# Kernel optimization log

Measured on AMD Instinct MI355X. Metric: run time of the kernel, lower is better.

## Reference

```python
import jax, jax.numpy as jnp
import numpy as np
from jax import lax

FILTERS = 8

def _conv(x, k):
    # x: (B,H,W,Cin), k: (KH,KW,Cin,Cout), SAME padding, stride 1
    return lax.conv_general_dilated(x, k, (1, 1), 'SAME',
                                    dimension_numbers=('NHWC', 'HWIO', 'NHWC'))

def _hard_sigmoid(x):
    # keras hard_sigmoid: clip(0.2*x + 0.5, 0, 1)
    return jnp.clip(0.2 * x + 0.5, 0.0, 1.0)


def setup_inputs() -> dict:
    key = jax.random.key(0)
    ks = jax.random.split(key, 4)
    B, T, H, W, C = 32, 16, 64, 64, 3
    x = jax.random.normal(ks[0], (B, T, H, W, C), dtype=jnp.float32)
    W_x = jax.random.normal(ks[1], (3, 3, C, 4 * FILTERS), dtype=jnp.float32) * 0.1
    W_h = jax.random.normal(ks[2], (3, 3, FILTERS, 4 * FILTERS), dtype=jnp.float32) * 0.1
    b = jnp.zeros((4 * FILTERS,), dtype=jnp.float32)
    W_out = jax.random.normal(ks[3], (H * W * FILTERS, 4), dtype=jnp.float32) * 0.02
    b_out = jnp.zeros((4,), dtype=jnp.float32)
    return {"x": x, "W_x": W_x, "W_h": W_h, "b": b, "W_out": W_out, "b_out": b_out}


def reference(x, W_x, W_h, b, W_out, b_out):
    B, T, H, W, C = x.shape
    F = FILTERS

    def step(carry, xt):
        h, c = carry
        z = _conv(xt, W_x) + _conv(h, W_h) + b  # (B,H,W,4F)
        zi, zf, zc, zo = jnp.split(z, 4, axis=-1)  # keras gate order: i, f, c, o
        i = _hard_sigmoid(zi)
        f = _hard_sigmoid(zf)
        c = f * c + i * jnp.tanh(zc)
        o = _hard_sigmoid(zo)
        h = o * jnp.tanh(c)
        return (h, c), None

    h0 = jnp.zeros((B, H, W, F), dtype=x.dtype)
    c0 = jnp.zeros((B, H, W, F), dtype=x.dtype)
    xs = jnp.moveaxis(x, 1, 0)  # (T,B,H,W,C)
    (h_final, _), _ = lax.scan(step, (h0, c0), xs)

    flat = h_final.reshape(B, -1)  # (B, H*W*F)
    logits = flat @ W_out + b_out
    return jax.nn.softmax(logits, axis=-1)
```

## Files before the change

kernel.cpp:

```cpp
#include <hip/hip_runtime.h>
#include <math.h>

#define NB 32
#define NT 16

typedef _Float16 f16;
typedef _Float16 half2f __attribute__((ext_vector_type(2)));
typedef _Float16 half4f __attribute__((ext_vector_type(4)));
typedef _Float16 half8f __attribute__((ext_vector_type(8)));
typedef float    floatx2 __attribute__((ext_vector_type(2)));
typedef float    floatx4 __attribute__((ext_vector_type(4)));

#define XPAD_OFF  0u
#define HPAD0_OFF 18382848u
#define HPAD1_OFF 20680704u
#define CBUF_OFF  22978560u
#define WBQ_OFF   27172864u
#define PART_OFF  27181056u
#define WS_NEED   27197440u

#define BANDA   0
#define BANDB   15232
#define CLDS4   30464
#define REDF4   55040
#define SMEM5   55296

__device__ __forceinline__ float hard_sigmoid(float v) {
    return fminf(fmaxf(fmaf(0.2f, v, 0.5f), 0.0f), 1.0f);
}
__device__ __forceinline__ float fast_tanh(float v) {
    float e = __builtin_amdgcn_exp2f(v * 2.8853900817779268f);
    return 1.0f - 2.0f * __builtin_amdgcn_rcpf(e + 1.0f);
}

__device__ __forceinline__ float wb_entry(int i, const float* Wx,
                                          const float* Wh, const float* bias) {
    int e = i & 7, l = (i >> 3) & 63, n = (i >> 9) & 1, j = i >> 10;
    int h = l >> 4;
    int rr = l & 15;
    int g = (rr & 3) * 8 + 2 * (rr >> 2) + n;
    float wv = 0.f;
    if (j == 0) {
        wv = Wh[(h * 8 + e) * 32 + g];
    } else if (j == 1) {
        wv = Wh[((4 + h) * 8 + e) * 32 + g];
    } else if (j == 2 && h == 0) {
        wv = Wh[(64 + e) * 32 + g];
    } else if (j == 3 && h == 3) {
        wv = (e == 3) ? bias[g] : 0.f;
    } else {
        int ty, txp;
        if (j == 2) { ty = (h == 3) ? 1 : 0; txp = (h == 2) ? 2 : 0; }
        else        { ty = (h == 0) ? 1 : 2; txp = (h == 1) ? 0 : 2; }
        int txq = txp + (e >> 2), c = e & 3;
        if (txq < 3 && c < 3)
            wv = Wx[((ty * 3 + txq) * 3 + c) * 32 + g];
    }
    return wv;
}

#define LDX(base, off) ({                                                  \
    half4f lo_ = *(const half4f*)((base) + (off));                         \
    half4f hi_ = *(const half4f*)((base) + (off) + 8);                     \
    __builtin_shufflevector(lo_, hi_, 0, 1, 2, 3, 4, 5, 6, 7); })

#define GATE_BODY(A0, A1, A2, A3, COLD0, COLD1, CC0, CC1, HH0, HH1)        \
    {                                                                      \
        floatx4 acc0 = {0.f, 0.f, 0.f, 0.f};                               \
        floatx4 acc1 = {0.f, 0.f, 0.f, 0.f};                               \
        acc0 = __builtin_amdgcn_mfma_f32_16x16x32_f16(B00, A0, acc0,0,0,0);\
        acc1 = __builtin_amdgcn_mfma_f32_16x16x32_f16(B01, A0, acc1,0,0,0);\
        acc0 = __builtin_amdgcn_mfma_f32_16x16x32_f16(B10, A1, acc0,0,0,0);\
        acc1 = __builtin_amdgcn_mfma_f32_16x16x32_f16(B11, A1, acc1,0,0,0);\
        acc0 = __builtin_amdgcn_mfma_f32_16x16x32_f16(B20, A2, acc0,0,0,0);\
        acc1 = __builtin_amdgcn_mfma_f32_16x16x32_f16(B21, A2, acc1,0,0,0);\
        acc0 = __builtin_amdgcn_mfma_f32_16x16x32_f16(B30, A3, acc0,0,0,0);\
        acc1 = __builtin_amdgcn_mfma_f32_16x16x32_f16(B31, A3, acc1,0,0,0);\
        float ig0 = hard_sigmoid(acc0[0]), fg0 = hard_sigmoid(acc0[1]);    \
        float cg0 = fast_tanh(acc0[2]),    og0 = hard_sigmoid(acc0[3]);    \
        CC0 = fmaf(fg0, COLD0, ig0 * cg0);                                 \
        HH0 = og0 * fast_tanh(CC0);                                        \
        float ig1 = hard_sigmoid(acc1[0]), fg1 = hard_sigmoid(acc1[1]);    \
        float cg1 = fast_tanh(acc1[2]),    og1 = hard_sigmoid(acc1[3]);    \
        CC1 = fmaf(fg1, COLD1, ig1 * cg1);                                 \
        HH1 = og1 * fast_tanh(CC1);                                        \
    }

__global__ __launch_bounds__(256) void init_all(
    const float* __restrict__ x,
    const float* __restrict__ Wx, const float* __restrict__ Wh,
    const float* __restrict__ bias,
    f16* __restrict__ xpad, f16* __restrict__ h0, f16* __restrict__ h1,
    f16* __restrict__ WB)
{
    int i = blockIdx.x * 256 + threadIdx.x;
    if (i < 200704) {
        int bt = i / 392, p = i - bt * 392;
        int rr, cc;
        if (p < 136) { rr = (p < 68) ? 0 : 65; cc = p - ((p < 68) ? 0 : 68); }
        else { int q = p - 136; rr = 1 + (q >> 2); int m = q & 3;
               cc = (m == 0) ? 0 : 64 + m; }
        half4f v = {0, 0, 0, (f16)1.0f};
        *(half4f*)(xpad + ((size_t)(bt * 66 + rr) * 68 + cc) * 4) = v;
    } else if (i < 225792) {
        int k = i - 200704;
        int buf = k / 12544; k -= buf * 12544;
        int b = k / 392, p = k - b * 392;
        int rr, cc;
        if (p < 136) { rr = (p < 68) ? 0 : 65; cc = p - ((p < 68) ? 0 : 68); }
        else { int q = p - 136; rr = 1 + (q >> 2); int m = q & 3;
               cc = (m == 0) ? 0 : 64 + m; }
        f16* hp = buf ? h1 : h0;
        half8f zz = {0, 0, 0, 0, 0, 0, 0, 0};
        *(half8f*)(hp + ((size_t)(b * 66 + rr) * 68 + cc) * 8) = zz;
    } else if (i < 229888) {
        int k = i - 225792;
        WB[k] = (f16)wb_entry(k, Wx, Wh, bias);
    } else if (i < 754176) {
        int j = i - 229888;
        int b = j >> 14;
        int rem = j & 16383;
        int s = rem >> 12, px = rem & 4095;
        const float* xp = x + ((size_t)(b * 16 + s) * 4096 + px) * 3;
        half4f v = {(f16)xp[0], (f16)xp[1], (f16)xp[2], (f16)1.0f};
        int gr = px >> 6, gc = px & 63;
        *(half4f*)(xpad + ((size_t)((b * 16 + s) * 66 + gr + 1) * 68 + gc + 1) * 4) = v;
    }
}

__global__ __launch_bounds__(1024, 4) void convlstm_fused4w(
    const float* __restrict__ x,
    f16* __restrict__ xpad,
    const f16* __restrict__ WB,
    const f16* __restrict__ h_in,
    f16* __restrict__ h_out,
    float* __restrict__ c_buf,
    const float* __restrict__ Wout,
    float* __restrict__ partial,
    int t, int first, int do_head)
{
    __shared__ __attribute__((aligned(16))) char smem[SMEM5];

    const int bid0 = blockIdx.x;
    const int bid  = ((bid0 & 7) << 5) | (bid0 >> 3);
    const int bi  = bid >> 3;
    const int r0  = (bid & 7) << 3;
    const int tid = threadIdx.x;
    const int w    = __builtin_amdgcn_readfirstlane(tid >> 6);
    const int lane = tid & 63;
    const int p16  = lane & 15;
    const int g4   = lane >> 4;
    const int f0   = g4 << 1;

    const int csl = t + 4 + (tid >> 8);
    const bool cv = (csl < NT);
    const int cpb = (tid & 255) << 1;
    const int cgr = r0 + (cpb >> 6), cgc = cpb & 63;
    float cxa0 = 0.f, cxa1 = 0.f, cxa2 = 0.f;
    float cxb0 = 0.f, cxb1 = 0.f, cxb2 = 0.f;
    if (cv) {
        const float* p = x + ((size_t)(bi * NT + csl) * 4096 + cgr * 64 + cgc) * 3;
        cxa0 = p[0]; cxa1 = p[1]; cxa2 = p[2];
        cxb0 = p[3]; cxb1 = p[4]; cxb2 = p[5];
    }

    const half8f* WBv = (const half8f*)WB;
    half8f B00 = WBv[0*64+lane], B01 = WBv[1*64+lane];
    half8f B10 = WBv[2*64+lane], B11 = WBv[3*64+lane];
    half8f B20 = WBv[4*64+lane], B21 = WBv[5*64+lane];
    half8f B30 = WBv[6*64+lane], B31 = WBv[7*64+lane];

    const int ty0 = (g4 >= 3) ? 1 : 0, tx0 = g4 - 3 * ty0;
    const int ty1 = 1 + ((g4 >= 2) ? 1 : 0), tx1 = (g4 + 4) - 3 * ty1;
    const int ty2 = (g4 == 3) ? 1 : 0, tx2 = (g4 == 2) ? 2 : 0;
    const int ty3 = (g4 == 0) ? 1 : 2, tx3 = (g4 == 1) ? 0 : 2;

    const half8f z8 = {0, 0, 0, 0, 0, 0, 0, 0};

    if (tid < 56) {
        int buf = tid / 28;
        int r2  = (tid % 28) >> 1;
        int cc  = (tid & 1) ? 65 : 0;
        *(half8f*)(smem + (buf ? BANDB : BANDA) + (r2 * 68 + cc) * 16) = z8;
    }

    #pragma unroll
    for (int k = 0; k < 4; ++k) {
        const int tau = k * 16 + w;
        if (tau < 56) {
            const int bl = tau >> 2, ct = tau & 3;
            const int row = r0 - 3 + bl;
            const bool vA = ((unsigned)row < 64u);
            const int colA = ct * 16 + p16;
            float cc0 = 0.f, cc1 = 0.f, hh0 = 0.f, hh1 = 0.f;
            if (vA) {
                floatx2 cold = {0.f, 0.f};
                if (!first)
                    cold = *(const floatx2*)(c_buf +
                               ((size_t)(bi * 4096 + row * 64 + colA)) * 8 + f0);
                const char* hpA = (const char*)(h_in + ((size_t)(bi * 66 + row)) * 68 * 8);
                const char* xpA = (const char*)(xpad +
                    ((size_t)((bi * 16 + t) * 66 + row)) * 68 * 4);
                half8f a0 = first ? z8 : *(const half8f*)(hpA + (ty0 * 68 + colA + tx0) * 16);
                half8f a1 = first ? z8 : *(const half8f*)(hpA + (ty1 * 68 + colA + tx1) * 16);
                half8f a2;
                if (g4 == 0) a2 = first ? z8 : *(const half8f*)(hpA + (2 * 68 + colA + 2) * 16);
                else         a2 = LDX(xpA, (ty2 * 68 + colA + tx2) * 8);
                half8f a3 = LDX(xpA, (ty3 * 68 + colA + tx3) * 8);
                GATE_BODY(a0, a1, a2, a3, cold[0], cold[1], cc0, cc1, hh0, hh1);
            }
            half2f hw = {(f16)hh0, (f16)hh1};
            *(half2f*)(smem + BANDA + (bl * 68 + 1 + colA) * 16 + f0 * 2) = hw;
            if (bl >= 1 && bl <= 12) {
                floatx2 cw = {cc0, cc1};
                *(floatx2*)(smem + CLDS4 + (((bl - 1) * 64 + colA) * 8 + f0) * 4) = cw;
            }
        }
    }
    __syncthreads();

    #pragma unroll
    for (int k = 0; k < 3; ++k) {
        const int tau = k * 16 + w;
        const int bl = 1 + (tau >> 2), ct = tau & 3;
        const int row = r0 - 3 + bl;
        const bool vA = ((unsigned)row < 64u);
        const int colA = ct * 16 + p16;
        float cc0 = 0.f, cc1 = 0.f, hh0 = 0.f, hh1 = 0.f;
        if (vA) {
            floatx2 cold = *(const floatx2*)(smem + CLDS4 +
                               (((bl - 1) * 64 + colA) * 8 + f0) * 4);
            const char* xpA = (const char*)(xpad +
                ((size_t)((bi * 16 + t + 1) * 66 + row)) * 68 * 4);
            half8f a0 = *(const half8f*)(smem + BANDA + ((bl - 1 + ty0) * 68 + colA + tx0) * 16);
            half8f a1 = *(const half8f*)(smem + BANDA + ((bl - 1 + ty1) * 68 + colA + tx1) * 16);
            half8f a2;
            if (g4 == 0) a2 = *(const half8f*)(smem + BANDA + ((bl + 1) * 68 + colA + 2) * 16);
            else         a2 = LDX(xpA, (ty2 * 68 + colA + tx2) * 8);
            half8f a3 = LDX(xpA, (ty3 * 68 + colA + tx3) * 8);
            GATE_BODY(a0, a1, a2, a3, cold[0], cold[1], cc0, cc1, hh0, hh1);
        }
        half2f hw = {(f16)hh0, (f16)hh1};
        *(half2f*)(smem + BANDB + (bl * 68 + 1 + colA) * 16 + f0 * 2) = hw;
        floatx2 cw = {cc0, cc1};
        *(floatx2*)(smem + CLDS4 + (((bl - 1) * 64 + colA) * 8 + f0) * 4) = cw;
    }
    __syncthreads();

    #pragma unroll
    for (int k = 0; k < 3; ++k) {
        const int tau = k * 16 + w;
        if (tau < 40) {
            const int bl = 2 + (tau >> 2), ct = tau & 3;
            const int row = r0 - 3 + bl;
            const bool vA = ((unsigned)row < 64u);
            const int colA = ct * 16 + p16;
            float cc0 = 0.f, cc1 = 0.f, hh0 = 0.f, hh1 = 0.f;
            if (vA) {
                floatx2 cold = *(const floatx2*)(smem + CLDS4 +
                                   (((bl - 1) * 64 + colA) * 8 + f0) * 4);
                const char* xpA = (const char*)(xpad +
                    ((size_t)((bi * 16 + t + 2) * 66 + row)) * 68 * 4);
                half8f a0 = *(const half8f*)(smem + BANDB + ((bl - 1 + ty0) * 68 + colA + tx0) * 16);
                half8f a1 = *(const half8f*)(smem + BANDB + ((bl - 1 + ty1) * 68 + colA + tx1) * 16);
                half8f a2;
                if (g4 == 0) a2 = *(const half8f*)(smem + BANDB + ((bl + 1) * 68 + colA + 2) * 16);
                else         a2 = LDX(xpA, (ty2 * 68 + colA + tx2) * 8);
                half8f a3 = LDX(xpA, (ty3 * 68 + colA + tx3) * 8);
                GATE_BODY(a0, a1, a2, a3, cold[0], cold[1], cc0, cc1, hh0, hh1);
            }
            half2f hw = {(f16)hh0, (f16)hh1};
            *(half2f*)(smem + BANDA + (bl * 68 + 1 + colA) * 16 + f0 * 2) = hw;
            floatx2 cw = {cc0, cc1};
            *(floatx2*)(smem + CLDS4 + (((bl - 1) * 64 + colA) * 8 + f0) * 4) = cw;
        }
    }
    __syncthreads();

    {
        float ha0 = 0.f, ha1 = 0.f, ha2 = 0.f, ha3 = 0.f;
        #pragma unroll
        for (int k = 0; k < 2; ++k) {
            const int tau = k * 16 + w;
            const int bl = 3 + (tau >> 2), ct = tau & 3;
            const int row = r0 - 3 + bl;
            const int colA = ct * 16 + p16;
            floatx2 cold = *(const floatx2*)(smem + CLDS4 +
                               (((bl - 1) * 64 + colA) * 8 + f0) * 4);
            const char* xpA = (const char*)(xpad +
                ((size_t)((bi * 16 + t + 3) * 66 + row)) * 68 * 4);
            half8f a0 = *(const half8f*)(smem + BANDA + ((bl - 1 + ty0) * 68 + colA + tx0) * 16);
            half8f a1 = *(const half8f*)(smem + BANDA + ((bl - 1 + ty1) * 68 + colA + tx1) * 16);
            half8f a2;
            if (g4 == 0) a2 = *(const half8f*)(smem + BANDA + ((bl + 1) * 68 + colA + 2) * 16);
            else         a2 = LDX(xpA, (ty2 * 68 + colA + tx2) * 8);
            half8f a3 = LDX(xpA, (ty3 * 68 + colA + tx3) * 8);
            float cc0, cc1, hh0, hh1;
            GATE_BODY(a0, a1, a2, a3, cold[0], cold[1], cc0, cc1, hh0, hh1);

            if (!do_head) {
                const size_t gp = (size_t)(bi * 4096 + row * 64 + colA);
                floatx2 cw = {cc0, cc1};
                *(floatx2*)(c_buf + gp * 8 + f0) = cw;
                const size_t hb = ((size_t)(bi * 66 + row + 1) * 68 + 1 + colA) * 8 + f0;
                half2f hw = {(f16)hh0, (f16)hh1};
                *(half2f*)(h_out + hb) = hw;
            } else {
                int pix = row * 64 + colA;
                floatx4 wa  = *(const floatx4*)(Wout + (size_t)(pix * 8 + f0) * 4);
                floatx4 wb2 = *(const floatx4*)(Wout + (size_t)(pix * 8 + f0 + 1) * 4);
                ha0 = fmaf(hh0, wa[0], fmaf(hh1, wb2[0], ha0));
                ha1 = fmaf(hh0, wa[1], fmaf(hh1, wb2[1], ha1));
                ha2 = fmaf(hh0, wa[2], fmaf(hh1, wb2[2], ha2));
                ha3 = fmaf(hh0, wa[3], fmaf(hh1, wb2[3], ha3));
            }
        }

        if (do_head) {
            #pragma unroll
            for (int off = 32; off >= 1; off >>= 1) {
                ha0 += __shfl_down(ha0, off, 64);
                ha1 += __shfl_down(ha1, off, 64);
                ha2 += __shfl_down(ha2, off, 64);
                ha3 += __shfl_down(ha3, off, 64);
            }
            if (lane == 0) {
                floatx4 v = {ha0, ha1, ha2, ha3};
                *(floatx4*)(smem + REDF4 + w * 16) = v;
            }
            __syncthreads();
            if (tid == 0) {
                floatx4 s = {0.f, 0.f, 0.f, 0.f};
                #pragma unroll
                for (int k = 0; k < 16; ++k)
                    s += *(const floatx4*)(smem + REDF4 + k * 16);
                *(floatx4*)(partial + (size_t)bid * 4) = s;
            }
        }
    }

    if (cv) {
        f16* dst = xpad + ((size_t)((bi * 16 + csl) * 66 + cgr + 1) * 68 + cgc + 1) * 4;
        half4f va = {(f16)cxa0, (f16)cxa1, (f16)cxa2, (f16)1.0f};
        half4f vb = {(f16)cxb0, (f16)cxb1, (f16)cxb2, (f16)1.0f};
        *(half4f*)(dst)     = va;
        *(half4f*)(dst + 4) = vb;
    }
}

__global__ __launch_bounds__(64) void head_finish(
    const float* __restrict__ partial,
    const float* __restrict__ bout,
    float* __restrict__ out)
{
    int b = threadIdx.x;
    if (b >= NB) return;
    float l0 = bout[0], l1 = bout[1], l2 = bout[2], l3 = bout[3];
    for (int s = 0; s < 8; ++s) {
        floatx4 p = *(const floatx4*)(partial + (size_t)(b * 8 + s) * 4);
        l0 += p[0]; l1 += p[1]; l2 += p[2]; l3 += p[3];
    }
    float m = fmaxf(fmaxf(l0, l1), fmaxf(l2, l3));
    float e0 = expf(l0 - m), e1 = expf(l1 - m);
    float e2 = expf(l2 - m), e3 = expf(l3 - m);
    float inv = 1.0f / (e0 + e1 + e2 + e3);
    out[b * 4 + 0] = e0 * inv;
    out[b * 4 + 1] = e1 * inv;
    out[b * 4 + 2] = e2 * inv;
    out[b * 4 + 3] = e3 * inv;
}

__global__ __launch_bounds__(256) void prepack_fb(
    const float* __restrict__ Wx, const float* __restrict__ Wh,
    const float* __restrict__ bias, f16* __restrict__ WB)
{
    int i = blockIdx.x * 256 + threadIdx.x;
    if (i < 4096) WB[i] = (f16)wb_entry(i, Wx, Wh, bias);
}

#define FB_XOFF 4352
#define FB_SMEM 6528

#define LDAS(off) ({                                                       \
    half4f lo_ = *(const half4f*)(smem + (off));                           \
    half4f hi_ = *(const half4f*)(smem + (off) + 8);                       \
    __builtin_shufflevector(lo_, hi_, 0, 1, 2, 3, 4, 5, 6, 7); })

__global__ __launch_bounds__(256, 4) void convlstm_step_fb(
    const float* __restrict__ x, const f16* __restrict__ WB,
    const f16* __restrict__ h_in, f16* __restrict__ h_out,
    float* __restrict__ c_buf, int t, int first)
{
    __shared__ __attribute__((aligned(16))) char smem[FB_SMEM];

    const int bid = blockIdx.x;
    const int bi  = bid >> 5;
    const int r0  = (bid & 31) << 1;
    const int tid = threadIdx.x;
    const int w    = tid >> 6;
    const int lane = tid & 63;
    const int p16  = lane & 15;
    const int g4   = lane >> 4;
    const int pr   = w >> 1;
    const int wcol = (w & 1) << 5;

    const float* xt = x + (((size_t)bi * NT + t) * 4096) * 3;

    for (int i = tid; i < 272; i += 256) {
        int lr = i / 68, lc = i - lr * 68;
        int gr = r0 - 1 + lr, gc = lc - 1;
        bool ok = ((unsigned)gr < 64u) && ((unsigned)gc < 64u);
        half4f xv = {0, 0, 0, (f16)1.0f};
        half8f hv = {0, 0, 0, 0, 0, 0, 0, 0};
        if (ok) {
            const float* xp = xt + (gr * 64 + gc) * 3;
            xv[0] = (f16)xp[0]; xv[1] = (f16)xp[1]; xv[2] = (f16)xp[2];
            if (!first)
                hv = *(const half8f*)(h_in + ((size_t)(bi * 4096 + gr * 64 + gc)) * 8);
        }
        *(half8f*)(smem + i * 16) = hv;
        *(half4f*)(smem + FB_XOFF + i * 8) = xv;
    }

    const half8f* WBv = (const half8f*)WB;
    half8f B00 = WBv[0*64+lane], B01 = WBv[1*64+lane];
    half8f B10 = WBv[2*64+lane], B11 = WBv[3*64+lane];
    half8f B20 = WBv[4*64+lane], B21 = WBv[5*64+lane];
    half8f B30 = WBv[6*64+lane], B31 = WBv[7*64+lane];

    const int f0 = g4 << 1;
    const size_t gp0 = (size_t)(bi * 4096 + (r0 + pr) * 64 + wcol + p16);
    const size_t gp1 = gp0 + 16;
    floatx2 cold0 = {0.f, 0.f}, cold1 = {0.f, 0.f};
    if (!first) {
        cold0 = *(const floatx2*)(c_buf + gp0 * 8 + f0);
        cold1 = *(const floatx2*)(c_buf + gp1 * 8 + f0);
    }

    __syncthreads();

    const int ty0 = (g4 >= 3) ? 1 : 0, tx0 = g4 - 3 * ty0;
    const int ty1 = 1 + ((g4 >= 2) ? 1 : 0), tx1 = (g4 + 4) - 3 * ty1;
    const int ty2 = (g4 == 3) ? 1 : 0, tx2 = (g4 == 2) ? 2 : 0;
    const int ty3 = (g4 == 0) ? 1 : 2, tx3 = (g4 == 1) ? 0 : 2;
    const int inc2 = (g4 == 0) ? 256 : 128;
    int o0 = ((pr + ty0) * 68 + wcol + p16 + tx0) * 16;
    int o1 = ((pr + ty1) * 68 + wcol + p16 + tx1) * 16;
    int o2 = (g4 == 0) ? ((pr + 2) * 68 + wcol + p16 + 2) * 16
                       : FB_XOFF + ((pr + ty2) * 68 + wcol + p16 + tx2) * 8;
    int o3 = FB_XOFF + ((pr + ty3) * 68 + wcol + p16 + tx3) * 8;

    #pragma unroll
    for (int tt = 0; tt < 2; ++tt) {
        half8f a0 = LDAS(o0), a1 = LDAS(o1), a2 = LDAS(o2), a3 = LDAS(o3);
        floatx2 cold = tt ? cold1 : cold0;
        float cc0, cc1, hh0, hh1;
        GATE_BODY(a0, a1, a2, a3, cold[0], cold[1], cc0, cc1, hh0, hh1);
        const size_t gp = tt ? gp1 : gp0;
        floatx2 cw = {cc0, cc1};
        *(floatx2*)(c_buf + gp * 8 + f0) = cw;
        half2f hw = {(f16)hh0, (f16)hh1};
        *(half2f*)(h_out + gp * 8 + f0) = hw;
        o0 += 256; o1 += 256; o2 += inc2; o3 += 128;
    }
}

__global__ __launch_bounds__(256) void head_partial_fb(
    const f16* __restrict__ h, const float* __restrict__ Wout,
    float* __restrict__ partial)
{
    const int b = blockIdx.x >> 4;
    const int chunk = blockIdx.x & 15;
    const int tid = threadIdx.x;
    const f16* hb = h + (size_t)b * 32768 + chunk * 2048;
    const float* wb = Wout + (size_t)(chunk * 2048) * 4;

    float acc[4] = {0.f, 0.f, 0.f, 0.f};
    #pragma unroll
    for (int it = 0; it < 8; ++it) {
        int i = it * 256 + tid;
        float hv = (float)hb[i];
        float4 wv = *(const float4*)(wb + (size_t)i * 4);
        acc[0] = fmaf(hv, wv.x, acc[0]);
        acc[1] = fmaf(hv, wv.y, acc[1]);
        acc[2] = fmaf(hv, wv.z, acc[2]);
        acc[3] = fmaf(hv, wv.w, acc[3]);
    }
    #pragma unroll
    for (int j = 0; j < 4; ++j)
        #pragma unroll
        for (int off = 32; off >= 1; off >>= 1)
            acc[j] += __shfl_down(acc[j], off, 64);

    __shared__ float red2[4][4];
    int lane = tid & 63, wv2 = tid >> 6;
    if (lane == 0) {
        #pragma unroll
        for (int j = 0; j < 4; ++j) red2[wv2][j] = acc[j];
    }
    __syncthreads();
    if (tid == 0) {
        #pragma unroll
        for (int j = 0; j < 4; ++j)
            partial[(size_t)blockIdx.x * 4 + j] =
                red2[0][j] + red2[1][j] + red2[2][j] + red2[3][j];
    }
}

__global__ __launch_bounds__(64) void head_finish_fb(
    const float* __restrict__ partial, const float* __restrict__ bout,
    float* __restrict__ out)
{
    int b = threadIdx.x;
    if (b >= NB) return;
    float logit[4] = {bout[0], bout[1], bout[2], bout[3]};
    #pragma unroll
    for (int k = 0; k < 16; ++k) {
        const float* p = partial + (size_t)(b * 16 + k) * 4;
        logit[0] += p[0]; logit[1] += p[1]; logit[2] += p[2]; logit[3] += p[3];
    }
    float m = fmaxf(fmaxf(logit[0], logit[1]), fmaxf(logit[2], logit[3]));
    float e[4], s = 0.f;
    #pragma unroll
    for (int j = 0; j < 4; ++j) { e[j] = expf(logit[j] - m); s += e[j]; }
    float inv = 1.0f / s;
    #pragma unroll
    for (int j = 0; j < 4; ++j) out[b * 4 + j] = e[j] * inv;
}

extern "C" void kernel_launch(void* const* d_in, const int* in_sizes, int n_in,
                              void* d_out, int out_size, void* d_ws, size_t ws_size,
                              hipStream_t stream) {
    const float* x    = (const float*)d_in[0];
    const float* Wx   = (const float*)d_in[1];
    const float* Wh   = (const float*)d_in[2];
    const float* b    = (const float*)d_in[3];
    const float* Wout = (const float*)d_in[4];
    const float* bout = (const float*)d_in[5];
    float* out = (float*)d_out;
    char* ws = (char*)d_ws;

    if (ws_size >= WS_NEED) {
        f16*   xpad  = (f16*)(ws + XPAD_OFF);
        f16*   h0    = (f16*)(ws + HPAD0_OFF);
        f16*   h1    = (f16*)(ws + HPAD1_OFF);
        float* cb    = (float*)(ws + CBUF_OFF);
        f16*   WBq   = (f16*)(ws + WBQ_OFF);
        float* part  = (float*)(ws + PART_OFF);

        init_all<<<2946, 256, 0, stream>>>(x, Wx, Wh, b, xpad, h0, h1, WBq);

        for (int k = 0; k < 4; ++k) {
            const f16* hin  = (k & 1) ? h0 : h1;
            f16*       hout = (k & 1) ? h1 : h0;
            convlstm_fused4w<<<256, 1024, 0, stream>>>(
                x, xpad, WBq, hin, hout, cb, Wout, part,
                4 * k, (k == 0) ? 1 : 0, (k == 3) ? 1 : 0);
        }
        head_finish<<<1, 64, 0, stream>>>(part, bout, out);
    } else {
        f16*   hA      = (f16*)ws;
        f16*   hB      = (f16*)(ws + (1u << 21));
        float* cb      = (float*)(ws + (1u << 22));
        f16*   WBq     = (f16*)(ws + (1u << 23));
        float* partial = (float*)(ws + (1u << 23) + 8192);

        prepack_fb<<<16, 256, 0, stream>>>(Wx, Wh, b, WBq);
        for (int t = 0; t < NT; ++t) {
            const f16* hin = (t & 1) ? hA : hB;
            f16*       hout = (t & 1) ? hB : hA;
            convlstm_step_fb<<<1024, 256, 0, stream>>>(x, WBq, hin, hout, cb,
                                                       t, (t == 0) ? 1 : 0);
        }
        head_partial_fb<<<512, 256, 0, stream>>>(hB, Wout, partial);
        head_finish_fb<<<1, 64, 0, stream>>>(partial, bout, out);
    }
}
```

Before: 65.77 us.

## Prefetch x-input fragments for later sub-steps early and pad cell-state LDS layout

Global loads of the padded input fragments for time sub-steps t+1..t+3 are hoisted into registers ahead of the preceding phase and barrier, so their latency overlaps earlier gate computation. The cell-state LDS buffer is also regrouped by g4 with a padded stride (CLG), which changes bank mapping and is likely meant to cut bank conflicts. This raises register pressure from the held half8f prefetch arrays, which may lower occupancy.

```diff
diff --git a/kernel.cpp b/kernel.cpp
--- a/kernel.cpp
+++ b/kernel.cpp
@@ -22,8 +22,11 @@
 #define BANDA   0
 #define BANDB   15232
 #define CLDS4   30464
-#define REDF4   55040
-#define SMEM5   55296
+#define CLG     6152
+#define REDF4   55072
+#define SMEM5   55328
+
+#define CLA(ci, col) (CLDS4 + g4 * CLG + (((ci) * 64 + (col)) * 8))
 
 __device__ __forceinline__ float hard_sigmoid(float v) {
     return fminf(fmaxf(fmaf(0.2f, v, 0.5f), 0.0f), 1.0f);
@@ -177,6 +180,19 @@
 
     const half8f z8 = {0, 0, 0, 0, 0, 0, 0, 0};
 
+    half8f p1x2[3], p1x3[3];
+    #pragma unroll
+    for (int k = 0; k < 3; ++k) {
+        const int tau = k * 16 + w;
+        const int bl = 1 + (tau >> 2), ct = tau & 3;
+        const int row = r0 - 3 + bl;
+        const int colA = ct * 16 + p16;
+        const char* xpA = (const char*)(xpad +
+            ((size_t)((bi * 16 + t + 1) * 66 + row)) * 68 * 4);
+        p1x2[k] = LDX(xpA, (ty2 * 68 + colA + tx2) * 8);
+        p1x3[k] = LDX(xpA, (ty3 * 68 + colA + tx3) * 8);
+    }
+
     if (tid < 56) {
         int buf = tid / 28;
         int r2  = (tid % 28) >> 1;
@@ -213,7 +229,7 @@
             *(half2f*)(smem + BANDA + (bl * 68 + 1 + colA) * 16 + f0 * 2) = hw;
             if (bl >= 1 && bl <= 12) {
                 floatx2 cw = {cc0, cc1};
-                *(floatx2*)(smem + CLDS4 + (((bl - 1) * 64 + colA) * 8 + f0) * 4) = cw;
+                *(floatx2*)(smem + CLA(bl - 1, colA)) = cw;
             }
         }
     }
@@ -228,22 +244,36 @@
         const int colA = ct * 16 + p16;
         float cc0 = 0.f, cc1 = 0.f, hh0 = 0.f, hh1 = 0.f;
         if (vA) {
-            floatx2 cold = *(const floatx2*)(smem + CLDS4 +
-                               (((bl - 1) * 64 + colA) * 8 + f0) * 4);
-            const char* xpA = (const char*)(xpad +
-                ((size_t)((bi * 16 + t + 1) * 66 + row)) * 68 * 4);
+            floatx2 cold = *(const floatx2*)(smem + CLA(bl - 1, colA));
             half8f a0 = *(const half8f*)(smem + BANDA + ((bl - 1 + ty0) * 68 + colA + tx0) * 16);
             half8f a1 = *(const half8f*)(smem + BANDA + ((bl - 1 + ty1) * 68 + colA + tx1) * 16);
-            half8f a2;
-            if (g4 == 0) a2 = *(const half8f*)(smem + BANDA + ((bl + 1) * 68 + colA + 2) * 16);
-            else         a2 = LDX(xpA, (ty2 * 68 + colA + tx2) * 8);
-            half8f a3 = LDX(xpA, (ty3 * 68 + colA + tx3) * 8);
+            half8f a2 = (g4 == 0)
+                ? *(const half8f*)(smem + BANDA + ((bl + 1) * 68 + colA + 2) * 16)
+                : p1x2[k];
+            half8f a3 = p1x3[k];
             GATE_BODY(a0, a1, a2, a3, cold[0], cold[1], cc0, cc1, hh0, hh1);
         }
         half2f hw = {(f16)hh0, (f16)hh1};
         *(half2f*)(smem + BANDB + (bl * 68 + 1 + colA) * 16 + f0 * 2) = hw;
         floatx2 cw = {cc0, cc1};
-        *(floatx2*)(smem + CLDS4 + (((bl - 1) * 64 + colA) * 8 + f0) * 4) = cw;
+        *(floatx2*)(smem + CLA(bl - 1, colA)) = cw;
+    }
+
+    half8f p2x2[3], p2x3[3];
+    #pragma unroll
+    for (int k = 0; k < 3; ++k) {
+        const int tau = k * 16 + w;
+        if (tau < 40) {
+            const int bl = 2 + (tau >> 2), ct = tau & 3;
+            const int row = r0 - 3 + bl;
+            const int colA = ct * 16 + p16;
+            const char* xpA = (const char*)(xpad +
+                ((size_t)((bi * 16 + t + 2) * 66 + row)) * 68 * 4);
+            p2x2[k] = LDX(xpA, (ty2 * 68 + colA + tx2) * 8);
+            p2x3[k] = LDX(xpA, (ty3 * 68 + colA + tx3) * 8);
+        } else {
+            p2x2[k] = z8; p2x3[k] = z8;
+        }
     }
     __syncthreads();
 
@@ -257,23 +287,33 @@
             const int colA = ct * 16 + p16;
             float cc0 = 0.f, cc1 = 0.f, hh0 = 0.f, hh1 = 0.f;
             if (vA) {
-                floatx2 cold = *(const floatx2*)(smem + CLDS4 +
-                                   (((bl - 1) * 64 + colA) * 8 + f0) * 4);
-                const char* xpA = (const char*)(xpad +
-                    ((size_t)((bi * 16 + t + 2) * 66 + row)) * 68 * 4);
+                floatx2 cold = *(const floatx2*)(smem + CLA(bl - 1, colA));
                 half8f a0 = *(const half8f*)(smem + BANDB + ((bl - 1 + ty0) * 68 + colA + tx0) * 16);
                 half8f a1 = *(const half8f*)(smem + BANDB + ((bl - 1 + ty1) * 68 + colA + tx1) * 16);
-                half8f a2;
-                if (g4 == 0) a2 = *(const half8f*)(smem + BANDB + ((bl + 1) * 68 + colA + 2) * 16);
-                else         a2 = LDX(xpA, (ty2 * 68 + colA + tx2) * 8);
-                half8f a3 = LDX(xpA, (ty3 * 68 + colA + tx3) * 8);
+                half8f a2 = (g4 == 0)
+                    ? *(const half8f*)(smem + BANDB + ((bl + 1) * 68 + colA + 2) * 16)
+                    : p2x2[k];
+                half8f a3 = p2x3[k];
                 GATE_BODY(a0, a1, a2, a3, cold[0], cold[1], cc0, cc1, hh0, hh1);
             }
             half2f hw = {(f16)hh0, (f16)hh1};
             *(half2f*)(smem + BANDA + (bl * 68 + 1 + colA) * 16 + f0 * 2) = hw;
             floatx2 cw = {cc0, cc1};
-            *(floatx2*)(smem + CLDS4 + (((bl - 1) * 64 + colA) * 8 + f0) * 4) = cw;
-        }
+            *(floatx2*)(smem + CLA(bl - 1, colA)) = cw;
+        }
+    }
+
+    half8f p3x2[2], p3x3[2];
+    #pragma unroll
+    for (int k = 0; k < 2; ++k) {
+        const int tau = k * 16 + w;
+        const int bl = 3 + (tau >> 2), ct = tau & 3;
+        const int row = r0 - 3 + bl;
+        const int colA = ct * 16 + p16;
+        const char* xpA = (const char*)(xpad +
+            ((size_t)((bi * 16 + t + 3) * 66 + row)) * 68 * 4);
+        p3x2[k] = LDX(xpA, (ty2 * 68 + colA + tx2) * 8);
+        p3x3[k] = LDX(xpA, (ty3 * 68 + colA + tx3) * 8);
     }
     __syncthreads();
 
@@ -285,16 +325,13 @@
             const int bl = 3 + (tau >> 2), ct = tau & 3;
             const int row = r0 - 3 + bl;
             const int colA = ct * 16 + p16;
-            floatx2 cold = *(const floatx2*)(smem + CLDS4 +
-                               (((bl - 1) * 64 + colA) * 8 + f0) * 4);
-            const char* xpA = (const char*)(xpad +
-                ((size_t)((bi * 16 + t + 3) * 66 + row)) * 68 * 4);
+            floatx2 cold = *(const floatx2*)(smem + CLA(bl - 1, colA));
             half8f a0 = *(const half8f*)(smem + BANDA + ((bl - 1 + ty0) * 68 + colA + tx0) * 16);
             half8f a1 = *(const half8f*)(smem + BANDA + ((bl - 1 + ty1) * 68 + colA + tx1) * 16);
-            half8f a2;
-            if (g4 == 0) a2 = *(const half8f*)(smem + BANDA + ((bl + 1) * 68 + colA + 2) * 16);
-            else         a2 = LDX(xpA, (ty2 * 68 + colA + tx2) * 8);
-            half8f a3 = LDX(xpA, (ty3 * 68 + colA + tx3) * 8);
+            half8f a2 = (g4 == 0)
+                ? *(const half8f*)(smem + BANDA + ((bl + 1) * 68 + colA + 2) * 16)
+                : p3x2[k];
+            half8f a3 = p3x3[k];
             float cc0, cc1, hh0, hh1;
             GATE_BODY(a0, a1, a2, a3, cold[0], cold[1], cc0, cc1, hh0, hh1);
 
```

Result: faster. 64.33 us, median of 2 (-2.2%).
